# Optimization experiments

Measured on AMD Instinct MI355X. Metric: run time of the kernel, lower is better.

The kernel has to match this reference:

```python
import jax, jax.numpy as jnp
import numpy as np

FACTOR = 5  # routing softmax power


def setup_inputs() -> dict:
    key = jax.random.key(0)
    kq, kk, kv = jax.random.split(key, 3)
    B, L, S, H, E, D = 2, 2048, 2048, 16, 64, 64
    queries = jax.random.normal(kq, (B, L, H, E), dtype=jnp.float32)
    keys = jax.random.normal(kk, (B, S, H, E), dtype=jnp.float32)
    values = jax.random.normal(kv, (B, S, H, D), dtype=jnp.float32)
    return {"queries": queries, "keys": keys, "values": values}


def reference(queries, keys, values):
    # NOTE: original computes scale = 1/sqrt(E) but never applies it; faithful.
    # Original computes the same unscaled QK^T twice; compute once and reuse.
    scores = jnp.einsum('blhe,bshe->bhls', queries, keys)  # [B,H,L,S]
    dense = jax.nn.softmax(scores, axis=-1)
    routing = dense ** FACTOR  # softmax(scores)**factor == routing_scores
    combined = (routing + dense) * 0.5
    sparse = combined / jnp.sum(combined, axis=-1, keepdims=True)
    V = jnp.einsum('bhls,bshd->blhd', sparse, values)  # [B,L,H,D]
    return V
```

## Files before the change

### kernel.cpp

```cpp
#include <hip/hip_runtime.h>
#include <math.h>


typedef _Float16 h8 __attribute__((ext_vector_type(8)));
typedef float f4 __attribute__((ext_vector_type(4)));
typedef float f16v __attribute__((ext_vector_type(16)));
typedef unsigned int u4v __attribute__((ext_vector_type(4)));

constexpr int Sc = 2048, Hc = 16;
constexpr int KB = 64, NT = Sc / KB;
constexpr float LOG2E = 1.4426950408889634f;

__device__ __forceinline__ f16v mm32(h8 a, h8 b, f16v c) {
  return __builtin_amdgcn_mfma_f32_32x32x16_f16(a, b, c, 0, 0, 0);
}
__device__ __forceinline__ unsigned pku(float a, float b) {
  return __builtin_bit_cast(unsigned, __builtin_amdgcn_cvt_pkrtz(a, b));
}

__global__ __launch_bounds__(256, 2) void dsa_mfma(
    const float* __restrict__ Q, const float* __restrict__ K,
    const float* __restrict__ V, float* __restrict__ O) {
  __shared__ __align__(16) _Float16 smem[4][2][64 * 64];

  const int tid = threadIdx.x;
  const int w = tid >> 6, lane = tid & 63, lm = lane & 31, hi = lane >> 5;
  const int swz = (lm & 7) << 3;

  const int blk = blockIdx.x;
  const int ww = (blk & 7) * 64 + (blk >> 3);
  const int qtb = ww & 15, bh = ww >> 4;
  const int b = bh >> 4, h = bh & 15;

  const size_t base = ((size_t)b * Sc * Hc + h) * 64;
  const float* Qb = Q + base;
  const float* Kb = K + base;
  const float* Vb = V + base;
  const int q0 = qtb * 128 + w * 32;

  h8 qf[4];
#pragma unroll
  for (int s = 0; s < 4; ++s) {
    const float* p = Qb + (size_t)(q0 + lm) * 1024 + s * 16 + hi * 8;
    f4 a = *(const f4*)p, c = *(const f4*)(p + 4);
#pragma unroll
    for (int i = 0; i < 4; ++i) {
      qf[s][i] = (_Float16)(a[i] * LOG2E);
      qf[s][4 + i] = (_Float16)(c[i] * LOG2E);
    }
  }
  h8 ones;
#pragma unroll
  for (int i = 0; i < 8; ++i) ones[i] = (_Float16)1.0f;

  f16v O1[2] = {}, O5[2] = {};
  f16v S1a = {}, S5a = {};
  float mr = -INFINITY;

  f4 kf[4];
  float vreg[2][8];
  const int krow = tid & 63, kq = tid >> 6;
  const int vd = tid & 63, vo0 = (tid >> 6) * 2;

  auto LOADK = [&](int k0) {
#pragma unroll
    for (int j = 0; j < 4; ++j)
      kf[j] = *(const f4*)(Kb + (size_t)(k0 + krow) * 1024 + kq * 16 + 4 * j);
  };
  auto LOADV = [&](int k0) {
#pragma unroll
    for (int i = 0; i < 2; ++i) {
      const float* p = Vb + (size_t)(k0 + (vo0 + i) * 8) * 1024 + vd;
#pragma unroll
      for (int j = 0; j < 8; ++j) vreg[i][j] = p[(size_t)j * 1024];
    }
  };
  auto STORE = [&](int buf) {
    _Float16* Ks = &smem[buf][0][0];
    _Float16* Vts = &smem[buf][1][0];
#pragma unroll
    for (int i = 0; i < 2; ++i) {
      u4v wv = {pku(kf[2 * i][0], kf[2 * i][1]), pku(kf[2 * i][2], kf[2 * i][3]),
                pku(kf[2 * i + 1][0], kf[2 * i + 1][1]), pku(kf[2 * i + 1][2], kf[2 * i + 1][3])};
      int col = (kq * 16 + 8 * i) ^ ((krow & 7) << 3);
      *(h8*)&Ks[krow * 64 + col] = __builtin_bit_cast(h8, wv);
    }
#pragma unroll
    for (int i = 0; i < 2; ++i) {
      u4v wv = {pku(vreg[i][0], vreg[i][1]), pku(vreg[i][2], vreg[i][3]),
                pku(vreg[i][4], vreg[i][5]), pku(vreg[i][6], vreg[i][7])};
      int col = ((vo0 + i) * 8) ^ ((vd & 7) << 3);
      *(h8*)&Vts[vd * 64 + col] = __builtin_bit_cast(h8, wv);
    }
  };

  auto QK = [&](int cur, f16v sc[2]) {
    const _Float16* Ks = &smem[cur][0][0];
    sc[0] = f16v{};
    sc[1] = f16v{};
    __builtin_amdgcn_s_setprio(1);
#pragma unroll
    for (int s = 0; s < 4; ++s) {
      h8 a0 = *(const h8*)&Ks[lm * 64 + ((s * 16 + hi * 8) ^ swz)];
      h8 a1 = *(const h8*)&Ks[(32 + lm) * 64 + ((s * 16 + hi * 8) ^ swz)];
      sc[0] = mm32(a0, qf[s], sc[0]);
      sc[1] = mm32(a1, qf[s], sc[1]);
    }
    __builtin_amdgcn_s_setprio(0);
  };

  auto PVX = [&](int cur, f16v sc[2]) {
    const _Float16* Vts = &smem[cur][1][0];
#pragma unroll
    for (int s = 0; s < 4; ++s) {
      const int kh = s >> 1, s8 = (s & 1) * 8;
      float e[8];
#pragma unroll
      for (int j = 0; j < 8; ++j) e[j] = __builtin_amdgcn_exp2f(sc[kh][s8 + j] - mr);
      auto rA = __builtin_amdgcn_permlane32_swap(pku(e[0], e[1]), pku(e[4], e[5]), false, false);
      auto rB = __builtin_amdgcn_permlane32_swap(pku(e[2], e[3]), pku(e[6], e[7]), false, false);
      u4v bwE = {(unsigned)rA[0], (unsigned)rB[0], (unsigned)rA[1], (unsigned)rB[1]};
      h8 bE = __builtin_bit_cast(h8, bwE);
      h8 b2 = bE * bE, b4 = b2 * b2, b5 = b4 * bE;

      h8 v0 = *(const h8*)&Vts[lm * 64 + ((s * 16 + hi * 8) ^ swz)];
      h8 v1 = *(const h8*)&Vts[(32 + lm) * 64 + ((s * 16 + hi * 8) ^ swz)];
      __builtin_amdgcn_s_setprio(1);
      O1[0] = mm32(v0, bE, O1[0]);
      O1[1] = mm32(v1, bE, O1[1]);
      S1a = mm32(ones, bE, S1a);
      O5[0] = mm32(v0, b5, O5[0]);
      O5[1] = mm32(v1, b5, O5[1]);
      S5a = mm32(ones, b5, S5a);
      __builtin_amdgcn_s_setprio(0);
    }
  };

  LOADK(0);
  LOADV(0);
  STORE(0);
  LOADK(KB);
  LOADV(KB);
  STORE(1);
  LOADK(2 * KB);
  LOADV(2 * KB);
  __syncthreads();

#pragma unroll 1
  for (int t = 0; t < NT; t += 2) {
    if (t + 2 < NT) STORE((t + 2) & 3);
    if (t + 3 < NT) {
      LOADK((t + 3) * KB);
      LOADV((t + 3) * KB);
    }

    f16v s0[2], s1[2];
    QK(t & 3, s0);
    QK((t + 1) & 3, s1);

    float m16[16];
#pragma unroll
    for (int r = 0; r < 16; ++r)
      m16[r] = fmaxf(fmaxf(s0[0][r], s0[1][r]), fmaxf(s1[0][r], s1[1][r]));
#pragma unroll
    for (int d = 8; d >= 1; d >>= 1)
#pragma unroll
      for (int r = 0; r < d; ++r) m16[r] = fmaxf(m16[r], m16[r + d]);
    float tm = fmaxf(m16[0], __shfl_xor(m16[0], 32));
    if (__any(tm > mr)) {
      float nm = fmaxf(mr, tm);
      float f = __builtin_amdgcn_exp2f(mr - nm);
      float f2 = f * f, f5 = f2 * f2 * f;
      mr = nm;
      S1a *= f;
      S5a *= f5;
#pragma unroll
      for (int dt = 0; dt < 2; ++dt) {
        O1[dt] *= f;
        O5[dt] *= f5;
      }
    }

    PVX(t & 3, s0);

    if (t + 3 < NT) STORE((t + 3) & 3);
    if (t + 4 < NT) {
      LOADK((t + 4) * KB);
      LOADV((t + 4) * KB);
    }

    PVX((t + 1) & 3, s1);

    __syncthreads();
  }

  const float z = S1a[0], z2 = z * z, z4 = z2 * z2;
  const float inv = 1.0f / (S5a[0] + z4 * S1a[0]);
#pragma unroll
  for (int dt = 0; dt < 2; ++dt)
#pragma unroll
    for (int i = 0; i < 4; ++i) {
      f4 o;
#pragma unroll
      for (int j = 0; j < 4; ++j)
        o[j] = (O5[dt][4 * i + j] + z4 * O1[dt][4 * i + j]) * inv;
      *(f4*)(O + base + (size_t)(q0 + lm) * 1024 + dt * 32 + 8 * i + 4 * hi) = o;
    }
}

extern "C" void kernel_launch(void* const* d_in, const int* in_sizes, int n_in,
                              void* d_out, int out_size, void* d_ws, size_t ws_size,
                              hipStream_t stream) {
  const float* q = (const float*)d_in[0];
  const float* k = (const float*)d_in[1];
  const float* v = (const float*)d_in[2];
  float* o = (float*)d_out;
  dsa_mfma<<<dim3(512), dim3(256), 0, stream>>>(q, k, v, o);
}
```

Baseline: 86.26 us.

## Replace ones-MFMA row sums with fdot2 and skip negligible power-5 MFMAs

Row sums of the softmax weights and their fifth powers are no longer computed with MFMAs against a ones matrix. Each lane now reduces its own values with packed fdot2 and combines the two half-waves with a shuffle at the end. The power-5 branch (b5 computation and its two MFMAs) is skipped for a tile pair when every query's tile max is more than 4.8 log2-units below the running max, because those terms then fall below fp16-level significance. This removes two of six MFMAs per sub-step, and more when the skip fires. In exchange it adds VALU dot work, a wave-wide vote per iteration, and a small approximation error in the skipped terms.

```diff
diff --git a/kernel.cpp b/kernel.cpp
--- a/kernel.cpp
+++ b/kernel.cpp
@@ -3,6 +3,8 @@
 
 
 typedef _Float16 h8 __attribute__((ext_vector_type(8)));
+typedef _Float16 h2 __attribute__((ext_vector_type(2)));
+typedef __fp16 g2 __attribute__((ext_vector_type(2)));
 typedef float f4 __attribute__((ext_vector_type(4)));
 typedef float f16v __attribute__((ext_vector_type(16)));
 typedef unsigned int u4v __attribute__((ext_vector_type(4)));
@@ -16,6 +18,9 @@
 }
 __device__ __forceinline__ unsigned pku(float a, float b) {
   return __builtin_bit_cast(unsigned, __builtin_amdgcn_cvt_pkrtz(a, b));
+}
+__device__ __forceinline__ float fdot2(h2 a, h2 b, float c) {
+  return __builtin_amdgcn_fdot2(__builtin_bit_cast(g2, a), __builtin_bit_cast(g2, b), c, false);
 }
 
 __global__ __launch_bounds__(256, 2) void dsa_mfma(
@@ -49,12 +54,10 @@
       qf[s][4 + i] = (_Float16)(c[i] * LOG2E);
     }
   }
-  h8 ones;
-#pragma unroll
-  for (int i = 0; i < 8; ++i) ones[i] = (_Float16)1.0f;
+  const h2 one2 = {(_Float16)1.0f, (_Float16)1.0f};
 
   f16v O1[2] = {}, O5[2] = {};
-  f16v S1a = {}, S5a = {};
+  float S1p[2] = {0.f, 0.f}, S5p[2] = {0.f, 0.f};
   float mr = -INFINITY;
 
   f4 kf[4];
@@ -109,11 +112,11 @@
     __builtin_amdgcn_s_setprio(0);
   };
 
-  auto PVX = [&](int cur, f16v sc[2]) {
+  auto PVX = [&](int cur, f16v sc[2], bool do5) {
     const _Float16* Vts = &smem[cur][1][0];
 #pragma unroll
     for (int s = 0; s < 4; ++s) {
-      const int kh = s >> 1, s8 = (s & 1) * 8;
+      const int kh = s >> 1, s8 = (s & 1) * 8, par = s & 1;
       float e[8];
 #pragma unroll
       for (int j = 0; j < 8; ++j) e[j] = __builtin_amdgcn_exp2f(sc[kh][s8 + j] - mr);
@@ -121,18 +124,35 @@
       auto rB = __builtin_amdgcn_permlane32_swap(pku(e[2], e[3]), pku(e[6], e[7]), false, false);
       u4v bwE = {(unsigned)rA[0], (unsigned)rB[0], (unsigned)rA[1], (unsigned)rB[1]};
       h8 bE = __builtin_bit_cast(h8, bwE);
-      h8 b2 = bE * bE, b4 = b2 * b2, b5 = b4 * bE;
+
+      float sp = fdot2(h2{bE[0], bE[1]}, one2, 0.f);
+      sp = fdot2(h2{bE[2], bE[3]}, one2, sp);
+      sp = fdot2(h2{bE[4], bE[5]}, one2, sp);
+      sp = fdot2(h2{bE[6], bE[7]}, one2, sp);
+      S1p[par] += sp;
 
       h8 v0 = *(const h8*)&Vts[lm * 64 + ((s * 16 + hi * 8) ^ swz)];
       h8 v1 = *(const h8*)&Vts[(32 + lm) * 64 + ((s * 16 + hi * 8) ^ swz)];
-      __builtin_amdgcn_s_setprio(1);
-      O1[0] = mm32(v0, bE, O1[0]);
-      O1[1] = mm32(v1, bE, O1[1]);
-      S1a = mm32(ones, bE, S1a);
-      O5[0] = mm32(v0, b5, O5[0]);
-      O5[1] = mm32(v1, b5, O5[1]);
-      S5a = mm32(ones, b5, S5a);
-      __builtin_amdgcn_s_setprio(0);
+
+      if (do5) {
+        h8 b2 = bE * bE, b4 = b2 * b2, b5 = b4 * bE;
+        float s5 = fdot2(h2{b5[0], b5[1]}, one2, 0.f);
+        s5 = fdot2(h2{b5[2], b5[3]}, one2, s5);
+        s5 = fdot2(h2{b5[4], b5[5]}, one2, s5);
+        s5 = fdot2(h2{b5[6], b5[7]}, one2, s5);
+        S5p[par] += s5;
+        __builtin_amdgcn_s_setprio(1);
+        O1[0] = mm32(v0, bE, O1[0]);
+        O1[1] = mm32(v1, bE, O1[1]);
+        O5[0] = mm32(v0, b5, O5[0]);
+        O5[1] = mm32(v1, b5, O5[1]);
+        __builtin_amdgcn_s_setprio(0);
+      } else {
+        __builtin_amdgcn_s_setprio(1);
+        O1[0] = mm32(v0, bE, O1[0]);
+        O1[1] = mm32(v1, bE, O1[1]);
+        __builtin_amdgcn_s_setprio(0);
+      }
     }
   };
 
@@ -172,16 +192,19 @@
       float f = __builtin_amdgcn_exp2f(mr - nm);
       float f2 = f * f, f5 = f2 * f2 * f;
       mr = nm;
-      S1a *= f;
-      S5a *= f5;
+      S1p[0] *= f;
+      S1p[1] *= f;
+      S5p[0] *= f5;
+      S5p[1] *= f5;
 #pragma unroll
       for (int dt = 0; dt < 2; ++dt) {
         O1[dt] *= f;
         O5[dt] *= f5;
       }
     }
-
-    PVX(t & 3, s0);
+    const bool do5 = __any(tm > mr - 4.8f);
+
+    PVX(t & 3, s0, do5);
 
     if (t + 3 < NT) STORE((t + 3) & 3);
     if (t + 4 < NT) {
@@ -189,13 +212,17 @@
       LOADV((t + 4) * KB);
     }
 
-    PVX((t + 1) & 3, s1);
+    PVX((t + 1) & 3, s1, do5);
 
     __syncthreads();
   }
 
-  const float z = S1a[0], z2 = z * z, z4 = z2 * z2;
-  const float inv = 1.0f / (S5a[0] + z4 * S1a[0]);
+  float S1 = S1p[0] + S1p[1];
+  S1 += __shfl_xor(S1, 32);
+  float S5 = S5p[0] + S5p[1];
+  S5 += __shfl_xor(S5, 32);
+  const float z = S1, z2 = z * z, z4 = z2 * z2;
+  const float inv = 1.0f / (S5 + z4 * S1);
 #pragma unroll
   for (int dt = 0; dt < 2; ++dt)
 #pragma unroll
```

Measured after the change: 113.3 us. 31.4% more time.
